# Kernel tuning notes

Measured on AMD Instinct MI355X. Metric: run time of the kernel, lower is better.

The kernel has to match this reference:

```python
import jax, jax.numpy as jnp
import numpy as np

N_NODES = 20000
N_EDGES = 320000
NUM_FEATURES = 128
CUTOFF = 5.0
NUM_RBF = 20
EPS = 1e-8


def setup_inputs() -> dict:
    key = jax.random.key(0)
    ks = jax.random.split(key, 10)
    v = jax.random.normal(ks[0], (N_NODES, NUM_FEATURES, 3), dtype=jnp.float32)
    s = jax.random.normal(ks[1], (N_NODES, NUM_FEATURES), dtype=jnp.float32)
    # edge list: col0 = src idx, col1 = dst idx (js), cols 2:5 = displacement vector
    src = jax.random.randint(ks[2], (N_EDGES,), 0, N_NODES).astype(jnp.float32)
    dst = jax.random.randint(ks[3], (N_EDGES,), 0, N_NODES).astype(jnp.float32)
    vec = jax.random.normal(ks[4], (N_EDGES, 3), dtype=jnp.float32) * 2.0
    r = jnp.concatenate([src[:, None], dst[:, None], vec], axis=1)
    # s_path params (torch Linear weight [out,in] -> stored here as [in,out])
    W1 = jax.random.normal(ks[5], (NUM_FEATURES, NUM_FEATURES), dtype=jnp.float32) * np.sqrt(2.0 / NUM_FEATURES)
    b1 = jnp.zeros((NUM_FEATURES,), dtype=jnp.float32)
    W2 = jax.random.normal(ks[6], (NUM_FEATURES, 3 * NUM_FEATURES), dtype=jnp.float32) * np.sqrt(2.0 / NUM_FEATURES)
    b2 = jnp.zeros((3 * NUM_FEATURES,), dtype=jnp.float32)
    # r_path params
    Wr = jax.random.normal(ks[7], (NUM_RBF, 3 * NUM_FEATURES), dtype=jnp.float32) * np.sqrt(1.0 / NUM_RBF)
    br = jnp.zeros((3 * NUM_FEATURES,), dtype=jnp.float32)
    return {"v": v, "s": s, "r": r, "W1": W1, "b1": b1, "W2": W2, "b2": b2, "Wr": Wr, "br": br}


def reference(v, s, r, W1, b1, W2, b2, Wr, br):
    nf = NUM_FEATURES
    js = r[:, 1].astype(jnp.int32)          # [E] destination node indices
    rv = r[:, 2:]                            # [E,3] displacement vectors

    # s_path: Linear -> SiLU -> Linear, computed per-node then gathered
    h = s @ W1 + b1
    phi = (h * jax.nn.sigmoid(h)) @ W2 + b2  # [N, 3*nf]

    # RBF expansion of edge distances
    norm_r = jnp.linalg.norm(rv, axis=1, keepdims=True)          # [E,1]
    norm_c = jnp.clip(norm_r, EPS)
    n = jnp.arange(1, NUM_RBF + 1, dtype=rv.dtype)[None, :]      # [1,20]
    rbf = jnp.clip(jnp.sin(n * (jnp.pi / CUTOFF) * norm_c) / (norm_c + EPS), -1.0, 1.0)

    # r_path Linear then cosine cutoff applied elementwise to the features
    Wf = rbf @ Wr + br                                            # [E, 3*nf]
    Wf = 0.5 * (jnp.cos(jnp.pi * Wf / CUTOFF) + 1.0) * (Wf < CUTOFF).astype(Wf.dtype)

    pre = phi[js, :] * Wf                                         # [E, 3*nf]
    split_1 = pre[:, :nf]
    split_2 = pre[:, nf:2 * nf]
    split_3 = pre[:, 2 * nf:]

    # NOTE: original code divides the normalized vector by the norm again
    rvn = rv / (norm_r + EPS)
    dir_term = rvn / (norm_r + EPS)                               # [E,3]
    left_2 = v[js, :, :] * split_1[:, :, None] + split_3[:, :, None] * dir_term[:, None, :]

    delta_v = jnp.zeros_like(v).at[js].add(left_2)
    delta_s = jnp.zeros_like(s).at[js].add(split_2)
    return (delta_v, delta_s)
```

## Files before the change

### kernel.cpp

```cpp
#include <hip/hip_runtime.h>
#include <math.h>

#define NND 20000
#define NE  320000
#define NF  128
#define NRBF 20
#define DEGCAP 48
#define SCATB 1250

typedef float f32x4 __attribute__((ext_vector_type(4)));
typedef short bf16x8 __attribute__((ext_vector_type(8)));

static constexpr float FEPS = 1e-8f;

__device__ __forceinline__ unsigned short f2bf(float x) {
    unsigned int u = __builtin_bit_cast(unsigned int, x);
    u += 0x7FFFu + ((u >> 16) & 1u);
    return (unsigned short)(u >> 16);
}
__device__ __forceinline__ float bf2f(unsigned short h) {
    unsigned int u = ((unsigned int)h) << 16;
    return __builtin_bit_cast(float, u);
}

__device__ __forceinline__ void pack_weights(int fid,
                                             const float* __restrict__ W1,
                                             const float* __restrict__ W2,
                                             const float* __restrict__ Wr,
                                             const float* __restrict__ br,
                                             unsigned short* __restrict__ Wp1,
                                             unsigned short* __restrict__ Wp2,
                                             unsigned short* __restrict__ WrP) {
    if (fid < 2048) {
        int lane = fid & 63, kk = (fid >> 6) & 3, nch = fid >> 8;
        int col = nch * 16 + (lane & 15);
        int k0 = kk * 32 + ((lane >> 4) * 8);
        unsigned short* o = Wp1 + (size_t)fid * 8;
#pragma unroll
        for (int j = 0; j < 8; j++) o[j] = f2bf(W1[(size_t)(k0 + j) * 128 + col]);
    } else if (fid < 2048 + 6144) {
        int f2 = fid - 2048;
        int lane = f2 & 63, kk = (f2 >> 6) & 3, nch = f2 >> 8;
        int col = nch * 16 + (lane & 15);
        int k0 = kk * 32 + ((lane >> 4) * 8);
        unsigned short* o = Wp2 + (size_t)f2 * 8;
#pragma unroll
        for (int j = 0; j < 8; j++) o[j] = f2bf(W2[(size_t)(k0 + j) * 384 + col]);
    } else if (fid < 2048 + 6144 + 1536) {
        int f3 = fid - 8192;
        int lane = f3 & 63, ft = f3 >> 6;
        int col = ft * 16 + (lane & 15);
        int k0 = (lane >> 4) * 8;
        unsigned short* o = WrP + (size_t)f3 * 8;
#pragma unroll
        for (int j = 0; j < 8; j++) {
            int k = k0 + j;
            float val;
            if (k < NRBF)            val = 0.1f * Wr[(size_t)k * 384 + col];
            else if (k == NRBF)      val = 0.1f * br[col];
            else if (k == NRBF + 1)  val = 1.0f;
            else                     val = 0.0f;
            o[j] = f2bf(val);
        }
    }
}

__device__ __forceinline__ void make_record(const float* __restrict__ re,
                                            unsigned short* __restrict__ rb,
                                            int& j) {
    j = (int)re[1];
    float x = re[2], y = re[3], z = re[4];
    float nrm = sqrtf(x * x + y * y + z * z);
    float nc = fmaxf(nrm, FEPS);
    float invd = 1.0f / (nc + FEPS);
    float inv2 = 1.0f / ((nrm + FEPS) * (nrm + FEPS));
#pragma unroll
    for (int k = 0; k < NRBF; k++) {
        float s0 = __builtin_amdgcn_sinf((float)(k + 1) * 0.1f * nc) * invd;
        rb[k] = f2bf(fminf(fmaxf(s0, -1.f), 1.f));
    }
    rb[20] = f2bf(x * inv2);
    rb[21] = f2bf(y * inv2);
    rb[22] = f2bf(z * inv2);
    rb[23] = 0;
}

__global__ __launch_bounds__(256) void prep_pad_k(const float* __restrict__ r,
                                                  int* __restrict__ cursor,
                                                  unsigned short* __restrict__ rec,
                                                  const float* __restrict__ W1,
                                                  const float* __restrict__ W2,
                                                  const float* __restrict__ Wr,
                                                  const float* __restrict__ br,
                                                  unsigned short* __restrict__ Wp1,
                                                  unsigned short* __restrict__ Wp2,
                                                  unsigned short* __restrict__ WrP) {
    if (blockIdx.x < SCATB) {
        int e = blockIdx.x * 256 + threadIdx.x;
        if (e >= NE) return;
        unsigned short rb[24];
        int j;
        make_record(r + (size_t)e * 5, rb, j);
        int pos = atomicAdd(&cursor[j], 1);
        if (pos < DEGCAP) {
            uint4* dst = (uint4*)(rec + ((size_t)j * DEGCAP + pos) * 24);
            const uint4* src = (const uint4*)rb;
            dst[0] = src[0]; dst[1] = src[1]; dst[2] = src[2];
        }
        return;
    }
    pack_weights((blockIdx.x - SCATB) * 256 + threadIdx.x, W1, W2, Wr, br, Wp1, Wp2, WrP);
}

__global__ __launch_bounds__(256) void histpack_k(const float* __restrict__ r,
                                                  int* __restrict__ counts,
                                                  const float* __restrict__ W1,
                                                  const float* __restrict__ W2,
                                                  const float* __restrict__ Wr,
                                                  const float* __restrict__ br,
                                                  unsigned short* __restrict__ Wp1,
                                                  unsigned short* __restrict__ Wp2,
                                                  unsigned short* __restrict__ WrP) {
    if (blockIdx.x < SCATB) {
        int e = blockIdx.x * 256 + threadIdx.x;
        if (e < NE) {
            int j = (int)r[(size_t)e * 5 + 1];
            atomicAdd(&counts[j], 1);
        }
        return;
    }
    pack_weights((blockIdx.x - SCATB) * 256 + threadIdx.x, W1, W2, Wr, br, Wp1, Wp2, WrP);
}

__global__ __launch_bounds__(1024) void scan_k(int* counts_cursor, int* offsets) {
    __shared__ int part[1024];
    const int CH = 20;
    int t = threadIdx.x;
    int base = t * CH;
    int loc[CH];
    int sum = 0;
#pragma unroll
    for (int i = 0; i < CH; i++) {
        int idx = base + i;
        int c = (idx < NND) ? counts_cursor[idx] : 0;
        loc[i] = sum;
        sum += c;
    }
    part[t] = sum;
    __syncthreads();
    for (int off = 1; off < 1024; off <<= 1) {
        int val = (t >= off) ? part[t - off] : 0;
        __syncthreads();
        part[t] += val;
        __syncthreads();
    }
    int excl = part[t] - sum;
#pragma unroll
    for (int i = 0; i < CH; i++) {
        int idx = base + i;
        if (idx < NND) {
            int o = excl + loc[i];
            offsets[idx] = o;
            counts_cursor[idx] = o;
        }
    }
    if (t == 1023) offsets[NND] = part[1023];
}

__global__ __launch_bounds__(256) void scatrec_k(const float* __restrict__ r,
                                                 int* __restrict__ cursor,
                                                 unsigned short* __restrict__ rec) {
    int e = blockIdx.x * 256 + threadIdx.x;
    if (e >= NE) return;
    unsigned short rb[24];
    int j;
    make_record(r + (size_t)e * 5, rb, j);
    int pos = atomicAdd(&cursor[j], 1);
    uint4* dst = (uint4*)(rec + (size_t)pos * 24);
    const uint4* src = (const uint4*)rb;
    dst[0] = src[0]; dst[1] = src[1]; dst[2] = src[2];
}

__global__ __launch_bounds__(64) void mlp_k(const float* __restrict__ s,
                                            const unsigned short* __restrict__ Wp1,
                                            const float* __restrict__ b1,
                                            const unsigned short* __restrict__ Wp2,
                                            const float* __restrict__ b2,
                                            unsigned short* __restrict__ phi) {
    __shared__ unsigned short lds[8192];
    int lane = threadIdx.x;
    int node0 = blockIdx.x * 16;
    int arow = lane & 15, kgrp = lane >> 4;
    unsigned short* hW = lds;
    unsigned short* pW = lds + 2048;

    int anode = node0 + arow; if (anode > NND - 1) anode = NND - 1;
    const float* ap = s + (size_t)anode * NF + kgrp * 8;
    bf16x8 afrag[4];
#pragma unroll
    for (int kk = 0; kk < 4; kk++) {
        float4 x0 = *(const float4*)(ap + kk * 32);
        float4 x1 = *(const float4*)(ap + kk * 32 + 4);
        union { unsigned short u[8]; bf16x8 v; } c;
        c.u[0] = f2bf(x0.x); c.u[1] = f2bf(x0.y); c.u[2] = f2bf(x0.z); c.u[3] = f2bf(x0.w);
        c.u[4] = f2bf(x1.x); c.u[5] = f2bf(x1.y); c.u[6] = f2bf(x1.z); c.u[7] = f2bf(x1.w);
        afrag[kk] = c.v;
    }
    f32x4 acc[8];
#pragma unroll
    for (int n = 0; n < 8; n++) acc[n] = (f32x4)(0.0f);
    const bf16x8* W8a = (const bf16x8*)Wp1;
#pragma unroll
    for (int nch = 0; nch < 8; nch++)
#pragma unroll
        for (int kk = 0; kk < 4; kk++)
            acc[nch] = __builtin_amdgcn_mfma_f32_16x16x32_bf16(
                afrag[kk], W8a[(nch * 4 + kk) * 64 + lane], acc[nch], 0, 0, 0);
#pragma unroll
    for (int nch = 0; nch < 8; nch++) {
        int col = nch * 16 + arow;
        float bb = b1[col];
#pragma unroll
        for (int rg = 0; rg < 4; rg++) {
            int row = kgrp * 4 + rg;
            float x = acc[nch][rg] + bb;
            float y = x / (1.0f + __expf(-x));
            hW[row * 128 + col] = f2bf(y);
        }
    }
    __syncthreads();
    bf16x8 hfrag[4];
#pragma unroll
    for (int kk = 0; kk < 4; kk++)
        hfrag[kk] = *(const bf16x8*)(hW + arow * 128 + kk * 32 + kgrp * 8);
#pragma unroll
    for (int c = 0; c < 3; c++) {
        f32x4 acc2[8];
#pragma unroll
        for (int n = 0; n < 8; n++) acc2[n] = (f32x4)(0.0f);
        const bf16x8* W8b = (const bf16x8*)Wp2;
#pragma unroll
        for (int nch = 0; nch < 8; nch++)
#pragma unroll
            for (int kk = 0; kk < 4; kk++)
                acc2[nch] = __builtin_amdgcn_mfma_f32_16x16x32_bf16(
                    hfrag[kk], W8b[((c * 8 + nch) * 4 + kk) * 64 + lane], acc2[nch], 0, 0, 0);
#pragma unroll
        for (int nch = 0; nch < 8; nch++) {
            int colg = c * 128 + nch * 16 + arow;
            float bb = b2[colg];
#pragma unroll
            for (int rg = 0; rg < 4; rg++) {
                int row = kgrp * 4 + rg;
                pW[row * 384 + colg] = f2bf(acc2[nch][rg] + bb);
            }
        }
    }
    __syncthreads();
#pragma unroll
    for (int it = 0; it < 12; it++) {
        int idx = it * 64 + lane;
        int row = idx / 48, ch = idx - row * 48;
        int node = node0 + row;
        if (node < NND) {
            uint4 val = *(const uint4*)(pW + row * 384 + ch * 8);
            *(uint4*)(phi + (size_t)node * 384 + ch * 8) = val;
        }
    }
}

template <bool PAD>
__global__ __launch_bounds__(256, 4) void reduce11_k(const int* __restrict__ offs_or_deg,
                                                     const unsigned short* __restrict__ rec,
                                                     const unsigned short* __restrict__ phi,
                                                     const float* __restrict__ v,
                                                     const unsigned short* __restrict__ WrP,
                                                     float* __restrict__ dv,
                                                     float* __restrict__ ds) {
    int tid = threadIdx.x;
    int lane = tid & 63;
    int la = lane & 15, kg = lane >> 4;
    int gwid = blockIdx.x * 4 + (tid >> 6);
    int w = gwid & 1;
    int jstart = gwid >> 1;
    int jstride = (gridDim.x * 4) >> 1;

    bool isKg2 = (kg == 2), isKg3 = (kg == 3);

    bf16x8 wrf[12];
#pragma unroll
    for (int q = 0; q < 12; q++)
        wrf[q] = *(const bf16x8*)(WrP + (size_t)(((2 * q + w) << 6) + lane) * 8);

    for (int j = jstart; j < NND; j += jstride) {
        int beg, deg;
        if (PAD) {
            beg = j * DEGCAP;
            deg = offs_or_deg[j]; if (deg > DEGCAP) deg = DEGCAP;
        } else {
            beg = offs_or_deg[j];
            deg = offs_or_deg[j + 1] - beg;
        }

        int f = (2 * kg + w) * 16 + la;
        const unsigned short* ph = phi + (size_t)j * 384;
        float p1 = bf2f(ph[f]), p2 = bf2f(ph[128 + f]), p3 = bf2f(ph[256 + f]);
        size_t vb = ((size_t)j * NF + f) * 3;
        float vx = v[vb], vy = v[vb + 1], vz = v[vb + 2];

        float a0[4], a1[4], sdx[4], sdy[4], sdz[4];
        float DX = 0.f, DY = 0.f, DZ = 0.f;
#pragma unroll
        for (int i = 0; i < 4; i++) { a0[i] = 0.f; a1[i] = 0.f; sdx[i] = 0.f; sdy[i] = 0.f; sdz[i] = 0.f; }

        int ntiles = (deg + 15) >> 4;
        uint4 c_next = make_uint4(0, 0, 0, 0);
        if (ntiles > 0 && !isKg3) {
            int idx = beg + (la < deg ? la : deg - 1);
            c_next = *(const uint4*)(rec + (size_t)idx * 24 + kg * 8);
        }

        for (int t5 = 0; t5 < ntiles; t5++) {
            uint4 c = c_next;
            if (t5 + 1 < ntiles && !isKg3) {
                int i2 = t5 * 16 + 16 + la;
                int idx = beg + (i2 < deg ? i2 : deg - 1);
                c_next = *(const uint4*)(rec + (size_t)idx * 24 + kg * 8);
            }
            int cnt = deg - t5 * 16; if (cnt > 16) cnt = 16;

            float dirx = bf2f((unsigned short)(c.z & 0xFFFF));
            float diry = bf2f((unsigned short)(c.z >> 16));
            float dirz = bf2f((unsigned short)(c.w & 0xFFFF));
            if (isKg2) {
                c.z = (la < cnt) ? 0x00003F80u : 0x41203F80u;
                c.w = 0u;
            }
            union { uint4 u; bf16x8 v8; } af;
            af.u = c;

            float dx[4], dy[4], dz[4];
#pragma unroll
            for (int rr = 0; rr < 4; rr++) {
                int er = kg * 4 + rr;
                dx[rr] = __shfl(dirx, 32 + er);
                dy[rr] = __shfl(diry, 32 + er);
                dz[rr] = __shfl(dirz, 32 + er);
            }
            DX += dx[0] + dx[1] + dx[2] + dx[3];
            DY += dy[0] + dy[1] + dy[2] + dy[3];
            DZ += dz[0] + dz[1] + dz[2] + dz[3];

#pragma unroll
            for (int q = 0; q < 12; q++) {
                f32x4 d = __builtin_amdgcn_mfma_f32_16x16x32_bf16(
                    af.v8, wrf[q], (f32x4)(0.0f), 0, 0, 0);
#pragma unroll
                for (int rr = 0; rr < 4; rr++) {
                    float t = __builtin_amdgcn_cosf(fminf(d[rr], 0.5f));
                    if (q < 4)      a0[q] += t;
                    else if (q < 8) a1[q - 4] += t;
                    else {
                        sdx[q - 8] = fmaf(t, dx[rr], sdx[q - 8]);
                        sdy[q - 8] = fmaf(t, dy[rr], sdy[q - 8]);
                        sdz[q - 8] = fmaf(t, dz[rr], sdz[q - 8]);
                    }
                }
            }
        }
#pragma unroll
        for (int i = 0; i < 4; i++) {
            a0[i] += __shfl_xor(a0[i], 16);  a0[i] += __shfl_xor(a0[i], 32);
            a1[i] += __shfl_xor(a1[i], 16);  a1[i] += __shfl_xor(a1[i], 32);
            sdx[i] += __shfl_xor(sdx[i], 16); sdx[i] += __shfl_xor(sdx[i], 32);
            sdy[i] += __shfl_xor(sdy[i], 16); sdy[i] += __shfl_xor(sdy[i], 32);
            sdz[i] += __shfl_xor(sdz[i], 16); sdz[i] += __shfl_xor(sdz[i], 32);
        }
        DX += __shfl_xor(DX, 16); DX += __shfl_xor(DX, 32);
        DY += __shfl_xor(DY, 16); DY += __shfl_xor(DY, 32);
        DZ += __shfl_xor(DZ, 16); DZ += __shfl_xor(DZ, 32);
        float R = (float)(ntiles << 4);

        float A0 = 0, A1 = 0, SX = 0, SY = 0, SZ = 0;
#pragma unroll
        for (int i = 0; i < 4; i++) {
            if (kg == i) { A0 = a0[i]; A1 = a1[i]; SX = sdx[i]; SY = sdy[i]; SZ = sdz[i]; }
        }
        float sum1 = 0.5f * (A0 + R);
        float sum2 = 0.5f * (A1 + R);
        float sx = 0.5f * (SX + DX);
        float sy = 0.5f * (SY + DY);
        float sz = 0.5f * (SZ + DZ);

        ds[(size_t)j * NF + f] = p2 * sum2;
        float c1 = p1 * sum1;
        dv[vb + 0] = fmaf(vx, c1, p3 * sx);
        dv[vb + 1] = fmaf(vy, c1, p3 * sy);
        dv[vb + 2] = fmaf(vz, c1, p3 * sz);
    }
}

extern "C" void kernel_launch(void* const* d_in, const int* in_sizes, int n_in,
                              void* d_out, int out_size, void* d_ws, size_t ws_size,
                              hipStream_t stream) {
    const float* v  = (const float*)d_in[0];
    const float* s  = (const float*)d_in[1];
    const float* r  = (const float*)d_in[2];
    const float* W1 = (const float*)d_in[3];
    const float* b1 = (const float*)d_in[4];
    const float* W2 = (const float*)d_in[5];
    const float* b2 = (const float*)d_in[6];
    const float* Wr = (const float*)d_in[7];
    const float* br = (const float*)d_in[8];

    float* dv = (float*)d_out;
    float* ds = dv + (size_t)NND * NF * 3;

    char* ws = (char*)d_ws;

    const size_t REC_PAD = (size_t)NND * DEGCAP * 48;
    const size_t PAD_NEED = 80128 + REC_PAD + 32768 + 98304 + 24576 + 15360000;

    if (ws_size >= PAD_NEED) {
        int* cursor             = (int*)ws;
        unsigned short* rec     = (unsigned short*)(ws + 80128);
        unsigned short* Wp1     = (unsigned short*)(ws + 80128 + REC_PAD);
        unsigned short* Wp2     = (unsigned short*)((char*)Wp1 + 32768);
        unsigned short* WrP     = (unsigned short*)((char*)Wp2 + 98304);
        unsigned short* phi     = (unsigned short*)((char*)WrP + 24576);

        hipMemsetAsync(cursor, 0, NND * sizeof(int), stream);
        prep_pad_k<<<SCATB + 38, 256, 0, stream>>>(r, cursor, rec,
                                                   W1, W2, Wr, br, Wp1, Wp2, WrP);
        mlp_k<<<(NND + 15) / 16, 64, 0, stream>>>(s, Wp1, b1, Wp2, b2, phi);
        reduce11_k<true><<<2560, 256, 0, stream>>>(cursor, rec, phi, v, WrP, dv, ds);
    } else {
        int* offsets            = (int*)ws;
        int* cursor             = (int*)(ws + 80128);
        unsigned short* rec     = (unsigned short*)(ws + 160256);
        unsigned short* Wp1     = (unsigned short*)(ws + 15520256);
        unsigned short* Wp2     = (unsigned short*)(ws + 15553024);
        unsigned short* WrP     = (unsigned short*)(ws + 15651328);
        unsigned short* phi     = (unsigned short*)(ws + 15675904);

        hipMemsetAsync(cursor, 0, NND * sizeof(int), stream);
        histpack_k<<<SCATB + 38, 256, 0, stream>>>(r, cursor, W1, W2, Wr, br, Wp1, Wp2, WrP);
        scan_k<<<1, 1024, 0, stream>>>(cursor, offsets);
        scatrec_k<<<(NE + 255) / 256, 256, 0, stream>>>(r, cursor, rec);
        mlp_k<<<(NND + 15) / 16, 64, 0, stream>>>(s, Wp1, b1, Wp2, b2, phi);
        reduce11_k<false><<<2560, 256, 0, stream>>>(offsets, rec, phi, v, WrP, dv, ds);
    }
}
```

Before: 105.9 us.

## Fuse edge scatter with node MLP launch and unroll reduce tile loop by two

Weight packing moves into its own small kernel. The edge-record scatter and the per-node MLP are merged into one launch, so the independent scatter and MLP blocks run concurrently instead of back to back. In the fused kernel each MLP block uses only 64 of 256 threads, and the block barriers are replaced by waitcnt, which is valid only because a single wavefront does the MLP work. The reduce kernel drops the occupancy hint from its launch bounds, and its software-prefetched tile loop becomes a two-tile unrolled loop that loads both records up front. This trades prefetch across iterations for more memory-level parallelism within each pair of tiles.

```diff
diff --git a/kernel.cpp b/kernel.cpp
--- a/kernel.cpp
+++ b/kernel.cpp
@@ -85,16 +85,113 @@
     rb[23] = 0;
 }
 
-__global__ __launch_bounds__(256) void prep_pad_k(const float* __restrict__ r,
-                                                  int* __restrict__ cursor,
-                                                  unsigned short* __restrict__ rec,
-                                                  const float* __restrict__ W1,
-                                                  const float* __restrict__ W2,
-                                                  const float* __restrict__ Wr,
-                                                  const float* __restrict__ br,
-                                                  unsigned short* __restrict__ Wp1,
-                                                  unsigned short* __restrict__ Wp2,
-                                                  unsigned short* __restrict__ WrP) {
+__global__ __launch_bounds__(256) void pack_k(const float* __restrict__ W1,
+                                              const float* __restrict__ W2,
+                                              const float* __restrict__ Wr,
+                                              const float* __restrict__ br,
+                                              unsigned short* __restrict__ Wp1,
+                                              unsigned short* __restrict__ Wp2,
+                                              unsigned short* __restrict__ WrP) {
+    pack_weights(blockIdx.x * 256 + threadIdx.x, W1, W2, Wr, br, Wp1, Wp2, WrP);
+}
+
+__device__ __forceinline__ void mlp_body(int node0, int lane,
+                                         unsigned short* __restrict__ lds,
+                                         const float* __restrict__ s,
+                                         const unsigned short* __restrict__ Wp1,
+                                         const float* __restrict__ b1,
+                                         const unsigned short* __restrict__ Wp2,
+                                         const float* __restrict__ b2,
+                                         unsigned short* __restrict__ phi) {
+    int arow = lane & 15, kgrp = lane >> 4;
+    unsigned short* hW = lds;
+    unsigned short* pW = lds + 2048;
+
+    int anode = node0 + arow; if (anode > NND - 1) anode = NND - 1;
+    const float* ap = s + (size_t)anode * NF + kgrp * 8;
+    bf16x8 afrag[4];
+#pragma unroll
+    for (int kk = 0; kk < 4; kk++) {
+        float4 x0 = *(const float4*)(ap + kk * 32);
+        float4 x1 = *(const float4*)(ap + kk * 32 + 4);
+        union { unsigned short u[8]; bf16x8 v; } c;
+        c.u[0] = f2bf(x0.x); c.u[1] = f2bf(x0.y); c.u[2] = f2bf(x0.z); c.u[3] = f2bf(x0.w);
+        c.u[4] = f2bf(x1.x); c.u[5] = f2bf(x1.y); c.u[6] = f2bf(x1.z); c.u[7] = f2bf(x1.w);
+        afrag[kk] = c.v;
+    }
+    f32x4 acc[8];
+#pragma unroll
+    for (int n = 0; n < 8; n++) acc[n] = (f32x4)(0.0f);
+    const bf16x8* W8a = (const bf16x8*)Wp1;
+#pragma unroll
+    for (int nch = 0; nch < 8; nch++)
+#pragma unroll
+        for (int kk = 0; kk < 4; kk++)
+            acc[nch] = __builtin_amdgcn_mfma_f32_16x16x32_bf16(
+                afrag[kk], W8a[(nch * 4 + kk) * 64 + lane], acc[nch], 0, 0, 0);
+#pragma unroll
+    for (int nch = 0; nch < 8; nch++) {
+        int col = nch * 16 + arow;
+        float bb = b1[col];
+#pragma unroll
+        for (int rg = 0; rg < 4; rg++) {
+            int row = kgrp * 4 + rg;
+            float x = acc[nch][rg] + bb;
+            float y = x / (1.0f + __expf(-x));
+            hW[row * 128 + col] = f2bf(y);
+        }
+    }
+    __builtin_amdgcn_s_waitcnt(0);
+    bf16x8 hfrag[4];
+#pragma unroll
+    for (int kk = 0; kk < 4; kk++)
+        hfrag[kk] = *(const bf16x8*)(hW + arow * 128 + kk * 32 + kgrp * 8);
+#pragma unroll
+    for (int c = 0; c < 3; c++) {
+        f32x4 acc2[8];
+#pragma unroll
+        for (int n = 0; n < 8; n++) acc2[n] = (f32x4)(0.0f);
+        const bf16x8* W8b = (const bf16x8*)Wp2;
+#pragma unroll
+        for (int nch = 0; nch < 8; nch++)
+#pragma unroll
+            for (int kk = 0; kk < 4; kk++)
+                acc2[nch] = __builtin_amdgcn_mfma_f32_16x16x32_bf16(
+                    hfrag[kk], W8b[((c * 8 + nch) * 4 + kk) * 64 + lane], acc2[nch], 0, 0, 0);
+#pragma unroll
+        for (int nch = 0; nch < 8; nch++) {
+            int colg = c * 128 + nch * 16 + arow;
+            float bb = b2[colg];
+#pragma unroll
+            for (int rg = 0; rg < 4; rg++) {
+                int row = kgrp * 4 + rg;
+                pW[row * 384 + colg] = f2bf(acc2[nch][rg] + bb);
+            }
+        }
+    }
+    __builtin_amdgcn_s_waitcnt(0);
+#pragma unroll
+    for (int it = 0; it < 12; it++) {
+        int idx = it * 64 + lane;
+        int row = idx / 48, ch = idx - row * 48;
+        int node = node0 + row;
+        if (node < NND) {
+            uint4 val = *(const uint4*)(pW + row * 384 + ch * 8);
+            *(uint4*)(phi + (size_t)node * 384 + ch * 8) = val;
+        }
+    }
+}
+
+__global__ __launch_bounds__(256) void scatmlp_k(const float* __restrict__ r,
+                                                 int* __restrict__ cursor,
+                                                 unsigned short* __restrict__ rec,
+                                                 const float* __restrict__ s,
+                                                 const unsigned short* __restrict__ Wp1,
+                                                 const float* __restrict__ b1,
+                                                 const unsigned short* __restrict__ Wp2,
+                                                 const float* __restrict__ b2,
+                                                 unsigned short* __restrict__ phi) {
+    __shared__ unsigned short lds[8192];
     if (blockIdx.x < SCATB) {
         int e = blockIdx.x * 256 + threadIdx.x;
         if (e >= NE) return;
@@ -109,7 +206,9 @@
         }
         return;
     }
-    pack_weights((blockIdx.x - SCATB) * 256 + threadIdx.x, W1, W2, Wr, br, Wp1, Wp2, WrP);
+    if (threadIdx.x >= 64) return;
+    int node0 = (blockIdx.x - SCATB) * 16;
+    mlp_body(node0, threadIdx.x, lds, s, Wp1, b1, Wp2, b2, phi);
 }
 
 __global__ __launch_bounds__(256) void histpack_k(const float* __restrict__ r,
@@ -188,95 +287,61 @@
                                             const float* __restrict__ b2,
                                             unsigned short* __restrict__ phi) {
     __shared__ unsigned short lds[8192];
-    int lane = threadIdx.x;
-    int node0 = blockIdx.x * 16;
-    int arow = lane & 15, kgrp = lane >> 4;
-    unsigned short* hW = lds;
-    unsigned short* pW = lds + 2048;
-
-    int anode = node0 + arow; if (anode > NND - 1) anode = NND - 1;
-    const float* ap = s + (size_t)anode * NF + kgrp * 8;
-    bf16x8 afrag[4];
-#pragma unroll
-    for (int kk = 0; kk < 4; kk++) {
-        float4 x0 = *(const float4*)(ap + kk * 32);
-        float4 x1 = *(const float4*)(ap + kk * 32 + 4);
-        union { unsigned short u[8]; bf16x8 v; } c;
-        c.u[0] = f2bf(x0.x); c.u[1] = f2bf(x0.y); c.u[2] = f2bf(x0.z); c.u[3] = f2bf(x0.w);
-        c.u[4] = f2bf(x1.x); c.u[5] = f2bf(x1.y); c.u[6] = f2bf(x1.z); c.u[7] = f2bf(x1.w);
-        afrag[kk] = c.v;
-    }
-    f32x4 acc[8];
-#pragma unroll
-    for (int n = 0; n < 8; n++) acc[n] = (f32x4)(0.0f);
-    const bf16x8* W8a = (const bf16x8*)Wp1;
-#pragma unroll
-    for (int nch = 0; nch < 8; nch++)
-#pragma unroll
-        for (int kk = 0; kk < 4; kk++)
-            acc[nch] = __builtin_amdgcn_mfma_f32_16x16x32_bf16(
-                afrag[kk], W8a[(nch * 4 + kk) * 64 + lane], acc[nch], 0, 0, 0);
-#pragma unroll
-    for (int nch = 0; nch < 8; nch++) {
-        int col = nch * 16 + arow;
-        float bb = b1[col];
-#pragma unroll
-        for (int rg = 0; rg < 4; rg++) {
-            int row = kgrp * 4 + rg;
-            float x = acc[nch][rg] + bb;
-            float y = x / (1.0f + __expf(-x));
-            hW[row * 128 + col] = f2bf(y);
-        }
-    }
-    __syncthreads();
-    bf16x8 hfrag[4];
-#pragma unroll
-    for (int kk = 0; kk < 4; kk++)
-        hfrag[kk] = *(const bf16x8*)(hW + arow * 128 + kk * 32 + kgrp * 8);
-#pragma unroll
-    for (int c = 0; c < 3; c++) {
-        f32x4 acc2[8];
-#pragma unroll
-        for (int n = 0; n < 8; n++) acc2[n] = (f32x4)(0.0f);
-        const bf16x8* W8b = (const bf16x8*)Wp2;
-#pragma unroll
-        for (int nch = 0; nch < 8; nch++)
-#pragma unroll
-            for (int kk = 0; kk < 4; kk++)
-                acc2[nch] = __builtin_amdgcn_mfma_f32_16x16x32_bf16(
-                    hfrag[kk], W8b[((c * 8 + nch) * 4 + kk) * 64 + lane], acc2[nch], 0, 0, 0);
-#pragma unroll
-        for (int nch = 0; nch < 8; nch++) {
-            int colg = c * 128 + nch * 16 + arow;
-            float bb = b2[colg];
-#pragma unroll
-            for (int rg = 0; rg < 4; rg++) {
-                int row = kgrp * 4 + rg;
-                pW[row * 384 + colg] = f2bf(acc2[nch][rg] + bb);
+    mlp_body(blockIdx.x * 16, threadIdx.x, lds, s, Wp1, b1, Wp2, b2, phi);
+}
+
+__device__ __forceinline__ void tile_rec(uint4 c, int cnt, int la, int kg,
+                                         bool isKg2, bool isKg3,
+                                         const bf16x8* __restrict__ wrf,
+                                         float* __restrict__ a0, float* __restrict__ a1,
+                                         float* __restrict__ sdx, float* __restrict__ sdy,
+                                         float* __restrict__ sdz,
+                                         float& DX, float& DY, float& DZ) {
+    float dirx = bf2f((unsigned short)(c.z & 0xFFFF));
+    float diry = bf2f((unsigned short)(c.z >> 16));
+    float dirz = bf2f((unsigned short)(c.w & 0xFFFF));
+    if (isKg2) {
+        c.z = (la < cnt) ? 0x00003F80u : 0x41203F80u;
+        c.w = 0u;
+    }
+    union { uint4 u; bf16x8 v8; } af;
+    af.u = c;
+    float dx[4], dy[4], dz[4];
+#pragma unroll
+    for (int rr = 0; rr < 4; rr++) {
+        int er = kg * 4 + rr;
+        dx[rr] = __shfl(dirx, 32 + er);
+        dy[rr] = __shfl(diry, 32 + er);
+        dz[rr] = __shfl(dirz, 32 + er);
+    }
+    DX += dx[0] + dx[1] + dx[2] + dx[3];
+    DY += dy[0] + dy[1] + dy[2] + dy[3];
+    DZ += dz[0] + dz[1] + dz[2] + dz[3];
+#pragma unroll
+    for (int q = 0; q < 12; q++) {
+        f32x4 d = __builtin_amdgcn_mfma_f32_16x16x32_bf16(af.v8, wrf[q], (f32x4)(0.0f), 0, 0, 0);
+#pragma unroll
+        for (int rr = 0; rr < 4; rr++) {
+            float t = __builtin_amdgcn_cosf(fminf(d[rr], 0.5f));
+            if (q < 4)      a0[q] += t;
+            else if (q < 8) a1[q - 4] += t;
+            else {
+                sdx[q - 8] = fmaf(t, dx[rr], sdx[q - 8]);
+                sdy[q - 8] = fmaf(t, dy[rr], sdy[q - 8]);
+                sdz[q - 8] = fmaf(t, dz[rr], sdz[q - 8]);
             }
         }
     }
-    __syncthreads();
-#pragma unroll
-    for (int it = 0; it < 12; it++) {
-        int idx = it * 64 + lane;
-        int row = idx / 48, ch = idx - row * 48;
-        int node = node0 + row;
-        if (node < NND) {
-            uint4 val = *(const uint4*)(pW + row * 384 + ch * 8);
-            *(uint4*)(phi + (size_t)node * 384 + ch * 8) = val;
-        }
-    }
 }
 
 template <bool PAD>
-__global__ __launch_bounds__(256, 4) void reduce11_k(const int* __restrict__ offs_or_deg,
-                                                     const unsigned short* __restrict__ rec,
-                                                     const unsigned short* __restrict__ phi,
-                                                     const float* __restrict__ v,
-                                                     const unsigned short* __restrict__ WrP,
-                                                     float* __restrict__ dv,
-                                                     float* __restrict__ ds) {
+__global__ __launch_bounds__(256) void reduce14_k(const int* __restrict__ offs_or_deg,
+                                                  const unsigned short* __restrict__ rec,
+                                                  const unsigned short* __restrict__ phi,
+                                                  const float* __restrict__ v,
+                                                  const unsigned short* __restrict__ WrP,
+                                                  float* __restrict__ dv,
+                                                  float* __restrict__ ds) {
     int tid = threadIdx.x;
     int lane = tid & 63;
     int la = lane & 15, kg = lane >> 4;
@@ -314,60 +379,31 @@
         for (int i = 0; i < 4; i++) { a0[i] = 0.f; a1[i] = 0.f; sdx[i] = 0.f; sdy[i] = 0.f; sdz[i] = 0.f; }
 
         int ntiles = (deg + 15) >> 4;
-        uint4 c_next = make_uint4(0, 0, 0, 0);
-        if (ntiles > 0 && !isKg3) {
-            int idx = beg + (la < deg ? la : deg - 1);
-            c_next = *(const uint4*)(rec + (size_t)idx * 24 + kg * 8);
-        }
-
-        for (int t5 = 0; t5 < ntiles; t5++) {
-            uint4 c = c_next;
-            if (t5 + 1 < ntiles && !isKg3) {
-                int i2 = t5 * 16 + 16 + la;
-                int idx = beg + (i2 < deg ? i2 : deg - 1);
-                c_next = *(const uint4*)(rec + (size_t)idx * 24 + kg * 8);
+        int t5 = 0;
+        for (; t5 + 2 <= ntiles; t5 += 2) {
+            uint4 cA = make_uint4(0, 0, 0, 0), cB = make_uint4(0, 0, 0, 0);
+            if (!isKg3) {
+                int iA = t5 * 16 + la;
+                int iB = (t5 + 1) * 16 + la;
+                iB = iB < deg ? iB : deg - 1;
+                cA = *(const uint4*)(rec + (size_t)(beg + iA) * 24 + kg * 8);
+                cB = *(const uint4*)(rec + (size_t)(beg + iB) * 24 + kg * 8);
+            }
+            int cntB = deg - (t5 + 1) * 16; if (cntB > 16) cntB = 16;
+            tile_rec(cA, 16, la, kg, isKg2, isKg3, wrf, a0, a1, sdx, sdy, sdz, DX, DY, DZ);
+            tile_rec(cB, cntB, la, kg, isKg2, isKg3, wrf, a0, a1, sdx, sdy, sdz, DX, DY, DZ);
+        }
+        if (t5 < ntiles) {
+            uint4 cA = make_uint4(0, 0, 0, 0);
+            if (!isKg3) {
+                int iA = t5 * 16 + la;
+                iA = iA < deg ? iA : deg - 1;
+                cA = *(const uint4*)(rec + (size_t)(beg + iA) * 24 + kg * 8);
             }
             int cnt = deg - t5 * 16; if (cnt > 16) cnt = 16;
-
-            float dirx = bf2f((unsigned short)(c.z & 0xFFFF));
-            float diry = bf2f((unsigned short)(c.z >> 16));
-            float dirz = bf2f((unsigned short)(c.w & 0xFFFF));
-            if (isKg2) {
-                c.z = (la < cnt) ? 0x00003F80u : 0x41203F80u;
-                c.w = 0u;
-            }
-            union { uint4 u; bf16x8 v8; } af;
-            af.u = c;
-
-            float dx[4], dy[4], dz[4];
-#pragma unroll
-            for (int rr = 0; rr < 4; rr++) {
-                int er = kg * 4 + rr;
-                dx[rr] = __shfl(dirx, 32 + er);
-                dy[rr] = __shfl(diry, 32 + er);
-                dz[rr] = __shfl(dirz, 32 + er);
-            }
-            DX += dx[0] + dx[1] + dx[2] + dx[3];
-            DY += dy[0] + dy[1] + dy[2] + dy[3];
-            DZ += dz[0] + dz[1] + dz[2] + dz[3];
-
-#pragma unroll
-            for (int q = 0; q < 12; q++) {
-                f32x4 d = __builtin_amdgcn_mfma_f32_16x16x32_bf16(
-                    af.v8, wrf[q], (f32x4)(0.0f), 0, 0, 0);
-#pragma unroll
-                for (int rr = 0; rr < 4; rr++) {
-                    float t = __builtin_amdgcn_cosf(fminf(d[rr], 0.5f));
-                    if (q < 4)      a0[q] += t;
-                    else if (q < 8) a1[q - 4] += t;
-                    else {
-                        sdx[q - 8] = fmaf(t, dx[rr], sdx[q - 8]);
-                        sdy[q - 8] = fmaf(t, dy[rr], sdy[q - 8]);
-                        sdz[q - 8] = fmaf(t, dz[rr], sdz[q - 8]);
-                    }
-                }
-            }
-        }
+            tile_rec(cA, cnt, la, kg, isKg2, isKg3, wrf, a0, a1, sdx, sdy, sdz, DX, DY, DZ);
+        }
+
 #pragma unroll
         for (int i = 0; i < 4; i++) {
             a0[i] += __shfl_xor(a0[i], 16);  a0[i] += __shfl_xor(a0[i], 32);
@@ -430,10 +466,10 @@
         unsigned short* phi     = (unsigned short*)((char*)WrP + 24576);
 
         hipMemsetAsync(cursor, 0, NND * sizeof(int), stream);
-        prep_pad_k<<<SCATB + 38, 256, 0, stream>>>(r, cursor, rec,
-                                                   W1, W2, Wr, br, Wp1, Wp2, WrP);
-        mlp_k<<<(NND + 15) / 16, 64, 0, stream>>>(s, Wp1, b1, Wp2, b2, phi);
-        reduce11_k<true><<<2560, 256, 0, stream>>>(cursor, rec, phi, v, WrP, dv, ds);
+        pack_k<<<38, 256, 0, stream>>>(W1, W2, Wr, br, Wp1, Wp2, WrP);
+        scatmlp_k<<<SCATB + (NND + 15) / 16, 256, 0, stream>>>(
+            r, cursor, rec, s, Wp1, b1, Wp2, b2, phi);
+        reduce14_k<true><<<2560, 256, 0, stream>>>(cursor, rec, phi, v, WrP, dv, ds);
     } else {
         int* offsets            = (int*)ws;
         int* cursor             = (int*)(ws + 80128);
@@ -448,6 +484,6 @@
         scan_k<<<1, 1024, 0, stream>>>(cursor, offsets);
         scatrec_k<<<(NE + 255) / 256, 256, 0, stream>>>(r, cursor, rec);
         mlp_k<<<(NND + 15) / 16, 64, 0, stream>>>(s, Wp1, b1, Wp2, b2, phi);
-        reduce11_k<false><<<2560, 256, 0, stream>>>(offsets, rec, phi, v, WrP, dv, ds);
-    }
-}
+        reduce14_k<false><<<2560, 256, 0, stream>>>(offsets, rec, phi, v, WrP, dv, ds);
+    }
+}
```

New measurement: 108.9 us. 2.8% more time.

## Fuse edge scatter with node MLP, fold memset into weight packing

Applied to the files above, without the earlier changes.

Weight packing moves into a small kernel that also zeroes the cursor array, which removes the separate memset. The edge-record scatter and the node MLP now share one launch, so the two independent stages can overlap. The MLP block runs one wave of a 256-thread block and swaps __syncthreads for a waitcnt, which is valid only because a single wave uses the LDS. The reduce kernel prefetches the next node's degree and drops the occupancy hint from its launch bounds. The cost is 192 idle threads and 16 KB of LDS per MLP block, plus possibly different register allocation in reduce.

```diff
diff --git a/kernel.cpp b/kernel.cpp
--- a/kernel.cpp
+++ b/kernel.cpp
@@ -85,16 +85,116 @@
     rb[23] = 0;
 }
 
-__global__ __launch_bounds__(256) void prep_pad_k(const float* __restrict__ r,
-                                                  int* __restrict__ cursor,
-                                                  unsigned short* __restrict__ rec,
-                                                  const float* __restrict__ W1,
-                                                  const float* __restrict__ W2,
-                                                  const float* __restrict__ Wr,
-                                                  const float* __restrict__ br,
-                                                  unsigned short* __restrict__ Wp1,
-                                                  unsigned short* __restrict__ Wp2,
-                                                  unsigned short* __restrict__ WrP) {
+__global__ __launch_bounds__(256) void pack_k(const float* __restrict__ W1,
+                                              const float* __restrict__ W2,
+                                              const float* __restrict__ Wr,
+                                              const float* __restrict__ br,
+                                              unsigned short* __restrict__ Wp1,
+                                              unsigned short* __restrict__ Wp2,
+                                              unsigned short* __restrict__ WrP,
+                                              int* __restrict__ cursor) {
+    int fid = blockIdx.x * 256 + threadIdx.x;
+    for (int i = fid; i < NND; i += gridDim.x * 256) cursor[i] = 0;
+    pack_weights(fid, W1, W2, Wr, br, Wp1, Wp2, WrP);
+}
+
+__device__ __forceinline__ void mlp_body(int node0, int lane,
+                                         unsigned short* __restrict__ lds,
+                                         const float* __restrict__ s,
+                                         const unsigned short* __restrict__ Wp1,
+                                         const float* __restrict__ b1,
+                                         const unsigned short* __restrict__ Wp2,
+                                         const float* __restrict__ b2,
+                                         unsigned short* __restrict__ phi) {
+    int arow = lane & 15, kgrp = lane >> 4;
+    unsigned short* hW = lds;
+    unsigned short* pW = lds + 2048;
+
+    int anode = node0 + arow; if (anode > NND - 1) anode = NND - 1;
+    const float* ap = s + (size_t)anode * NF + kgrp * 8;
+    bf16x8 afrag[4];
+#pragma unroll
+    for (int kk = 0; kk < 4; kk++) {
+        float4 x0 = *(const float4*)(ap + kk * 32);
+        float4 x1 = *(const float4*)(ap + kk * 32 + 4);
+        union { unsigned short u[8]; bf16x8 v; } c;
+        c.u[0] = f2bf(x0.x); c.u[1] = f2bf(x0.y); c.u[2] = f2bf(x0.z); c.u[3] = f2bf(x0.w);
+        c.u[4] = f2bf(x1.x); c.u[5] = f2bf(x1.y); c.u[6] = f2bf(x1.z); c.u[7] = f2bf(x1.w);
+        afrag[kk] = c.v;
+    }
+    f32x4 acc[8];
+#pragma unroll
+    for (int n = 0; n < 8; n++) acc[n] = (f32x4)(0.0f);
+    const bf16x8* W8a = (const bf16x8*)Wp1;
+#pragma unroll
+    for (int nch = 0; nch < 8; nch++)
+#pragma unroll
+        for (int kk = 0; kk < 4; kk++)
+            acc[nch] = __builtin_amdgcn_mfma_f32_16x16x32_bf16(
+                afrag[kk], W8a[(nch * 4 + kk) * 64 + lane], acc[nch], 0, 0, 0);
+#pragma unroll
+    for (int nch = 0; nch < 8; nch++) {
+        int col = nch * 16 + arow;
+        float bb = b1[col];
+#pragma unroll
+        for (int rg = 0; rg < 4; rg++) {
+            int row = kgrp * 4 + rg;
+            float x = acc[nch][rg] + bb;
+            float y = x / (1.0f + __expf(-x));
+            hW[row * 128 + col] = f2bf(y);
+        }
+    }
+    __builtin_amdgcn_s_waitcnt(0);
+    bf16x8 hfrag[4];
+#pragma unroll
+    for (int kk = 0; kk < 4; kk++)
+        hfrag[kk] = *(const bf16x8*)(hW + arow * 128 + kk * 32 + kgrp * 8);
+#pragma unroll
+    for (int c = 0; c < 3; c++) {
+        f32x4 acc2[8];
+#pragma unroll
+        for (int n = 0; n < 8; n++) acc2[n] = (f32x4)(0.0f);
+        const bf16x8* W8b = (const bf16x8*)Wp2;
+#pragma unroll
+        for (int nch = 0; nch < 8; nch++)
+#pragma unroll
+            for (int kk = 0; kk < 4; kk++)
+                acc2[nch] = __builtin_amdgcn_mfma_f32_16x16x32_bf16(
+                    hfrag[kk], W8b[((c * 8 + nch) * 4 + kk) * 64 + lane], acc2[nch], 0, 0, 0);
+#pragma unroll
+        for (int nch = 0; nch < 8; nch++) {
+            int colg = c * 128 + nch * 16 + arow;
+            float bb = b2[colg];
+#pragma unroll
+            for (int rg = 0; rg < 4; rg++) {
+                int row = kgrp * 4 + rg;
+                pW[row * 384 + colg] = f2bf(acc2[nch][rg] + bb);
+            }
+        }
+    }
+    __builtin_amdgcn_s_waitcnt(0);
+#pragma unroll
+    for (int it = 0; it < 12; it++) {
+        int idx = it * 64 + lane;
+        int row = idx / 48, ch = idx - row * 48;
+        int node = node0 + row;
+        if (node < NND) {
+            uint4 val = *(const uint4*)(pW + row * 384 + ch * 8);
+            *(uint4*)(phi + (size_t)node * 384 + ch * 8) = val;
+        }
+    }
+}
+
+__global__ __launch_bounds__(256) void scatmlp_k(const float* __restrict__ r,
+                                                 int* __restrict__ cursor,
+                                                 unsigned short* __restrict__ rec,
+                                                 const float* __restrict__ s,
+                                                 const unsigned short* __restrict__ Wp1,
+                                                 const float* __restrict__ b1,
+                                                 const unsigned short* __restrict__ Wp2,
+                                                 const float* __restrict__ b2,
+                                                 unsigned short* __restrict__ phi) {
+    __shared__ unsigned short lds[8192];
     if (blockIdx.x < SCATB) {
         int e = blockIdx.x * 256 + threadIdx.x;
         if (e >= NE) return;
@@ -109,7 +209,9 @@
         }
         return;
     }
-    pack_weights((blockIdx.x - SCATB) * 256 + threadIdx.x, W1, W2, Wr, br, Wp1, Wp2, WrP);
+    if (threadIdx.x >= 64) return;
+    int node0 = (blockIdx.x - SCATB) * 16;
+    mlp_body(node0, threadIdx.x, lds, s, Wp1, b1, Wp2, b2, phi);
 }
 
 __global__ __launch_bounds__(256) void histpack_k(const float* __restrict__ r,
@@ -188,95 +290,17 @@
                                             const float* __restrict__ b2,
                                             unsigned short* __restrict__ phi) {
     __shared__ unsigned short lds[8192];
-    int lane = threadIdx.x;
-    int node0 = blockIdx.x * 16;
-    int arow = lane & 15, kgrp = lane >> 4;
-    unsigned short* hW = lds;
-    unsigned short* pW = lds + 2048;
-
-    int anode = node0 + arow; if (anode > NND - 1) anode = NND - 1;
-    const float* ap = s + (size_t)anode * NF + kgrp * 8;
-    bf16x8 afrag[4];
-#pragma unroll
-    for (int kk = 0; kk < 4; kk++) {
-        float4 x0 = *(const float4*)(ap + kk * 32);
-        float4 x1 = *(const float4*)(ap + kk * 32 + 4);
-        union { unsigned short u[8]; bf16x8 v; } c;
-        c.u[0] = f2bf(x0.x); c.u[1] = f2bf(x0.y); c.u[2] = f2bf(x0.z); c.u[3] = f2bf(x0.w);
-        c.u[4] = f2bf(x1.x); c.u[5] = f2bf(x1.y); c.u[6] = f2bf(x1.z); c.u[7] = f2bf(x1.w);
-        afrag[kk] = c.v;
-    }
-    f32x4 acc[8];
-#pragma unroll
-    for (int n = 0; n < 8; n++) acc[n] = (f32x4)(0.0f);
-    const bf16x8* W8a = (const bf16x8*)Wp1;
-#pragma unroll
-    for (int nch = 0; nch < 8; nch++)
-#pragma unroll
-        for (int kk = 0; kk < 4; kk++)
-            acc[nch] = __builtin_amdgcn_mfma_f32_16x16x32_bf16(
-                afrag[kk], W8a[(nch * 4 + kk) * 64 + lane], acc[nch], 0, 0, 0);
-#pragma unroll
-    for (int nch = 0; nch < 8; nch++) {
-        int col = nch * 16 + arow;
-        float bb = b1[col];
-#pragma unroll
-        for (int rg = 0; rg < 4; rg++) {
-            int row = kgrp * 4 + rg;
-            float x = acc[nch][rg] + bb;
-            float y = x / (1.0f + __expf(-x));
-            hW[row * 128 + col] = f2bf(y);
-        }
-    }
-    __syncthreads();
-    bf16x8 hfrag[4];
-#pragma unroll
-    for (int kk = 0; kk < 4; kk++)
-        hfrag[kk] = *(const bf16x8*)(hW + arow * 128 + kk * 32 + kgrp * 8);
-#pragma unroll
-    for (int c = 0; c < 3; c++) {
-        f32x4 acc2[8];
-#pragma unroll
-        for (int n = 0; n < 8; n++) acc2[n] = (f32x4)(0.0f);
-        const bf16x8* W8b = (const bf16x8*)Wp2;
-#pragma unroll
-        for (int nch = 0; nch < 8; nch++)
-#pragma unroll
-            for (int kk = 0; kk < 4; kk++)
-                acc2[nch] = __builtin_amdgcn_mfma_f32_16x16x32_bf16(
-                    hfrag[kk], W8b[((c * 8 + nch) * 4 + kk) * 64 + lane], acc2[nch], 0, 0, 0);
-#pragma unroll
-        for (int nch = 0; nch < 8; nch++) {
-            int colg = c * 128 + nch * 16 + arow;
-            float bb = b2[colg];
-#pragma unroll
-            for (int rg = 0; rg < 4; rg++) {
-                int row = kgrp * 4 + rg;
-                pW[row * 384 + colg] = f2bf(acc2[nch][rg] + bb);
-            }
-        }
-    }
-    __syncthreads();
-#pragma unroll
-    for (int it = 0; it < 12; it++) {
-        int idx = it * 64 + lane;
-        int row = idx / 48, ch = idx - row * 48;
-        int node = node0 + row;
-        if (node < NND) {
-            uint4 val = *(const uint4*)(pW + row * 384 + ch * 8);
-            *(uint4*)(phi + (size_t)node * 384 + ch * 8) = val;
-        }
-    }
+    mlp_body(blockIdx.x * 16, threadIdx.x, lds, s, Wp1, b1, Wp2, b2, phi);
 }
 
 template <bool PAD>
-__global__ __launch_bounds__(256, 4) void reduce11_k(const int* __restrict__ offs_or_deg,
-                                                     const unsigned short* __restrict__ rec,
-                                                     const unsigned short* __restrict__ phi,
-                                                     const float* __restrict__ v,
-                                                     const unsigned short* __restrict__ WrP,
-                                                     float* __restrict__ dv,
-                                                     float* __restrict__ ds) {
+__global__ __launch_bounds__(256) void reduce15_k(const int* __restrict__ offs_or_deg,
+                                                  const unsigned short* __restrict__ rec,
+                                                  const unsigned short* __restrict__ phi,
+                                                  const float* __restrict__ v,
+                                                  const unsigned short* __restrict__ WrP,
+                                                  float* __restrict__ dv,
+                                                  float* __restrict__ ds) {
     int tid = threadIdx.x;
     int lane = tid & 63;
     int la = lane & 15, kg = lane >> 4;
@@ -292,11 +316,16 @@
     for (int q = 0; q < 12; q++)
         wrf[q] = *(const bf16x8*)(WrP + (size_t)(((2 * q + w) << 6) + lane) * 8);
 
+    int degN = 0;
+    if (jstart < NND) degN = PAD ? offs_or_deg[jstart] : 0;
+
     for (int j = jstart; j < NND; j += jstride) {
         int beg, deg;
         if (PAD) {
             beg = j * DEGCAP;
-            deg = offs_or_deg[j]; if (deg > DEGCAP) deg = DEGCAP;
+            deg = degN; if (deg > DEGCAP) deg = DEGCAP;
+            int jn = j + jstride;
+            if (jn < NND) degN = offs_or_deg[jn];
         } else {
             beg = offs_or_deg[j];
             deg = offs_or_deg[j + 1] - beg;
@@ -429,11 +458,10 @@
         unsigned short* WrP     = (unsigned short*)((char*)Wp2 + 98304);
         unsigned short* phi     = (unsigned short*)((char*)WrP + 24576);
 
-        hipMemsetAsync(cursor, 0, NND * sizeof(int), stream);
-        prep_pad_k<<<SCATB + 38, 256, 0, stream>>>(r, cursor, rec,
-                                                   W1, W2, Wr, br, Wp1, Wp2, WrP);
-        mlp_k<<<(NND + 15) / 16, 64, 0, stream>>>(s, Wp1, b1, Wp2, b2, phi);
-        reduce11_k<true><<<2560, 256, 0, stream>>>(cursor, rec, phi, v, WrP, dv, ds);
+        pack_k<<<38, 256, 0, stream>>>(W1, W2, Wr, br, Wp1, Wp2, WrP, cursor);
+        scatmlp_k<<<SCATB + (NND + 15) / 16, 256, 0, stream>>>(
+            r, cursor, rec, s, Wp1, b1, Wp2, b2, phi);
+        reduce15_k<true><<<2560, 256, 0, stream>>>(cursor, rec, phi, v, WrP, dv, ds);
     } else {
         int* offsets            = (int*)ws;
         int* cursor             = (int*)(ws + 80128);
@@ -448,6 +476,6 @@
         scan_k<<<1, 1024, 0, stream>>>(cursor, offsets);
         scatrec_k<<<(NE + 255) / 256, 256, 0, stream>>>(r, cursor, rec);
         mlp_k<<<(NND + 15) / 16, 64, 0, stream>>>(s, Wp1, b1, Wp2, b2, phi);
-        reduce11_k<false><<<2560, 256, 0, stream>>>(offsets, rec, phi, v, WrP, dv, ds);
-    }
-}
+        reduce15_k<false><<<2560, 256, 0, stream>>>(offsets, rec, phi, v, WrP, dv, ds);
+    }
+}
```

Result: faster. 98.29 us (-7.2%).
